# Kernel tuning notes

Measured on AMD Instinct MI355X. Metric: run time of the kernel, lower is better.

The kernel has to match this reference:

```python
import jax, jax.numpy as jnp
import numpy as np

V = 256; D = 512; H = 4 * 2; L = 4; B = 4; T = 512; ML = 1024
FF = 4 * D; FS = 256; NMEL = 80; PN = 512
H = 8


def _ghost(x, idx, scale, lut):
    # LUT dequant (gather) + per-row scale, then GEMM: y = x @ (lut[idx]*scale).T
    w = lut[idx] * scale
    return x @ w.T


def _ln(x, g, b, eps=1e-5):
    m = jnp.mean(x, axis=-1, keepdims=True)
    v = jnp.var(x, axis=-1, keepdims=True)
    return (x - m) / jnp.sqrt(v + eps) * g + b


def _conv1d(x, w, b, pad):
    # x: [B, C, T], w: [O, I, K]
    y = jax.lax.conv_general_dilated(x, w, (1,), [(pad, pad)],
                                     dimension_numbers=('NCH', 'OIH', 'NCH'))
    return y + b[None, :, None]


def _block(x, ai, asc, ui, usc, di, dsc, g, bb, lut):
    Bq, Tq, C = x.shape
    hd = C // H
    h = _ln(x, g[0], bb[0])
    q = _ghost(h, ai[0], asc[0], lut).reshape(Bq, Tq, H, hd).transpose(0, 2, 1, 3)
    k = _ghost(h, ai[1], asc[1], lut).reshape(Bq, Tq, H, hd).transpose(0, 2, 1, 3)
    v = _ghost(h, ai[2], asc[2], lut).reshape(Bq, Tq, H, hd).transpose(0, 2, 1, 3)
    att = jax.nn.softmax(jnp.einsum('bhqd,bhkd->bhqk', q, k) / float(np.sqrt(hd)), axis=-1)
    o = jnp.einsum('bhqk,bhkd->bhqd', att, v).transpose(0, 2, 1, 3).reshape(Bq, Tq, C)
    x = x + _ghost(o, ai[3], asc[3], lut)
    h = _ln(x, g[1], bb[1])
    h = jax.nn.gelu(_ghost(h, ui, usc, lut), approximate=False)
    return x + _ghost(h, di, dsc, lut)


def _varpred(x, p):
    c1w, c1b, g1, b1, c2w, c2b, g2, b2, lw, lb = p
    h = jax.nn.relu(_conv1d(x.transpose(0, 2, 1), c1w, c1b, 1)).transpose(0, 2, 1)
    h = _ln(h, g1, b1)
    h = jax.nn.relu(_conv1d(h.transpose(0, 2, 1), c2w, c2b, 1)).transpose(0, 2, 1)
    h = _ln(h, g2, b2)
    return (h @ lw.T + lb)[..., 0]


def _length_reg(x, dur, max_len):
    # repeat_interleave via cumsum + searchsorted, padded to fixed max_len
    def one(xi, di):
        c = jnp.cumsum(di)
        frames = jnp.arange(max_len)
        tok = jnp.searchsorted(c, frames, side='right')
        valid = (frames < c[-1]).astype(xi.dtype)[:, None]
        return xi[jnp.clip(tok, 0, xi.shape[0] - 1)] * valid
    return jax.vmap(one)(x, dur)


def _forward(floats, ints):
    (lut, emb_table, pos_table, dec_pos_table,
     e_as, e_us, e_ds, e_g, e_b,
     d_as, d_us, d_ds, d_g, d_b,
     vp_c1w, vp_c1b, vp_g1, vp_b1, vp_c2w, vp_c2b, vp_g2, vp_b2, vp_lw, vp_lb,
     proj_w, proj_b, mel_w, mel_b,
     pn_w1, pn_b1, pn_w2, pn_b2, pn_w3, pn_b3, pn_w4, pn_b4, pn_w5, pn_b5,
     pn_g, pn_bb) = floats
    (text, duration_target, e_ai, e_ui, e_di, d_ai, d_ui, d_di) = ints
    Tq = text.shape[1]
    x = emb_table[text] + pos_table[:Tq]
    for i in range(L):
        x = _block(x, e_ai[i], e_as[i], e_ui[i], e_us[i], e_di[i], e_ds[i], e_g[i], e_b[i], lut)
    vp = lambda j: (vp_c1w[j], vp_c1b[j], vp_g1[j], vp_b1[j], vp_c2w[j], vp_c2b[j],
                    vp_g2[j], vp_b2[j], vp_lw[j], vp_lb[j])
    dur_pred = _varpred(x, vp(0))
    x = _length_reg(x, duration_target, ML)
    pitch = _varpred(x, vp(1))
    x = x + pitch[..., None] * proj_w[0, :, 0] + proj_b[0]
    energy = _varpred(x, vp(2))
    x = x + energy[..., None] * proj_w[1, :, 0] + proj_b[1]
    x = x + dec_pos_table[:ML]
    for i in range(L):
        x = _block(x, d_ai[i], d_as[i], d_ui[i], d_us[i], d_di[i], d_ds[i], d_g[i], d_b[i], lut)
    mel = x @ mel_w.T + mel_b  # [B, ML, 80]
    h = mel.transpose(0, 2, 1)
    inv = float(1.0 / np.sqrt(1.0 + 1e-5))  # BN eval with running mean 0, var 1
    bn = lambda z, j: z * inv * pn_g[j][:, None] + pn_bb[j][:, None]
    for j, (w, b) in enumerate([(pn_w1, pn_b1), (pn_w2, pn_b2), (pn_w3, pn_b3), (pn_w4, pn_b4)]):
        h = jnp.tanh(bn(_conv1d(h, w, b, 2), j))
    h = _conv1d(h, pn_w5, pn_b5, 2)
    mel_post = mel + h.transpose(0, 2, 1)
    return mel, mel_post, dur_pred, pitch, energy


def setup_inputs():
    ks = iter(jax.random.split(jax.random.key(0), 80))
    nk = lambda: next(ks)
    lo, hi = -0.08, 0.08
    lut = jnp.linspace(lo, hi, 256, dtype=jnp.float32)
    def qidx(shape):
        w = jax.random.normal(nk(), shape, dtype=jnp.float32) * 0.02
        return jnp.clip(jnp.round((w - lo) / ((hi - lo) / 255.0)), 0, 255).astype(jnp.int32)
    rn = lambda shape, s=0.02: jax.random.normal(nk(), shape, dtype=jnp.float32) * s
    inp = {
        'text': jax.random.randint(nk(), (B, T), 0, V),
        'duration_target': jax.random.randint(nk(), (B, T), 0, 4),
        'lut': lut,
        'emb_table': rn((V, D)), 'pos_table': rn((1024, D)), 'dec_pos_table': rn((2048, D)),
        'e_ai': qidx((L, 4, D, D)), 'e_as': jnp.ones((L, 4, D, 1)),
        'e_ui': qidx((L, FF, D)), 'e_us': jnp.ones((L, FF, 1)),
        'e_di': qidx((L, D, FF)), 'e_ds': jnp.ones((L, D, 1)),
        'e_g': jnp.ones((L, 2, D)), 'e_b': jnp.zeros((L, 2, D)),
        'd_ai': qidx((L, 4, D, D)), 'd_as': jnp.ones((L, 4, D, 1)),
        'd_ui': qidx((L, FF, D)), 'd_us': jnp.ones((L, FF, 1)),
        'd_di': qidx((L, D, FF)), 'd_ds': jnp.ones((L, D, 1)),
        'd_g': jnp.ones((L, 2, D)), 'd_b': jnp.zeros((L, 2, D)),
        'vp_c1w': rn((3, FS, D, 3)), 'vp_c1b': jnp.zeros((3, FS)),
        'vp_g1': jnp.ones((3, FS)), 'vp_b1': jnp.zeros((3, FS)),
        'vp_c2w': rn((3, FS, FS, 3)), 'vp_c2b': jnp.zeros((3, FS)),
        'vp_g2': jnp.ones((3, FS)), 'vp_b2': jnp.zeros((3, FS)),
        'vp_lw': rn((3, 1, FS)), 'vp_lb': jnp.zeros((3, 1)),
        'proj_w': rn((2, D, 1)), 'proj_b': jnp.zeros((2, D)),
        'mel_w': rn((NMEL, D)), 'mel_b': jnp.zeros((NMEL,)),
        'pn_w1': rn((PN, NMEL, 5)), 'pn_b1': jnp.zeros((PN,)),
        'pn_w2': rn((PN, PN, 5)), 'pn_b2': jnp.zeros((PN,)),
        'pn_w3': rn((PN, PN, 5)), 'pn_b3': jnp.zeros((PN,)),
        'pn_w4': rn((PN, PN, 5)), 'pn_b4': jnp.zeros((PN,)),
        'pn_w5': rn((NMEL, PN, 5)), 'pn_b5': jnp.zeros((NMEL,)),
        'pn_g': jnp.ones((4, PN)), 'pn_bb': jnp.zeros((4, PN)),
    }
    return inp


def reference(text, duration_target, lut, emb_table, pos_table, dec_pos_table,
              e_ai, e_as, e_ui, e_us, e_di, e_ds, e_g, e_b,
              d_ai, d_as, d_ui, d_us, d_di, d_ds, d_g, d_b,
              vp_c1w, vp_c1b, vp_g1, vp_b1, vp_c2w, vp_c2b, vp_g2, vp_b2, vp_lw, vp_lb,
              proj_w, proj_b, mel_w, mel_b,
              pn_w1, pn_b1, pn_w2, pn_b2, pn_w3, pn_b3, pn_w4, pn_b4, pn_w5, pn_b5,
              pn_g, pn_bb):
    floats = (lut, emb_table, pos_table, dec_pos_table,
              e_as, e_us, e_ds, e_g, e_b,
              d_as, d_us, d_ds, d_g, d_b,
              vp_c1w, vp_c1b, vp_g1, vp_b1, vp_c2w, vp_c2b, vp_g2, vp_b2, vp_lw, vp_lb,
              proj_w, proj_b, mel_w, mel_b,
              pn_w1, pn_b1, pn_w2, pn_b2, pn_w3, pn_b3, pn_w4, pn_b4, pn_w5, pn_b5,
              pn_g, pn_bb)
    ints = (text, duration_target, e_ai, e_ui, e_di, d_ai, d_ui, d_di)
    return _forward(floats, ints)
```

## Files before the change

kernel.cpp:

```cpp
#include <hip/hip_runtime.h>
#include <math.h>

#define B_    4
#define T_ENC 512
#define ML_   1024
#define D_    512
#define H_    8
#define HD_   64
#define FF_   2048
#define FS_   256
#define NMEL_ 80
#define PN_   512
#define L_    4
#define QKVSTRIDE_ 2097152

typedef __attribute__((ext_vector_type(8))) short bf16x8;
typedef __attribute__((ext_vector_type(8))) unsigned short u16x8;
typedef __attribute__((ext_vector_type(4))) float f32x4;

__device__ inline unsigned short f2bf(float f) {
    union { float f; unsigned u; } v; v.f = f;
    unsigned r = (v.u + 0x7FFFu + ((v.u >> 16) & 1u)) >> 16;
    return (unsigned short)r;
}

__global__ void embed_kernel(const int* __restrict__ text, const float* __restrict__ emb,
                             const float* __restrict__ pos, float* __restrict__ x) {
    int row = blockIdx.x;
    int t = row % T_ENC;
    int tok = text[row];
    float4 e = ((const float4*)(emb + (size_t)tok * D_))[threadIdx.x];
    float4 p = ((const float4*)(pos + (size_t)t * D_))[threadIdx.x];
    e.x += p.x; e.y += p.y; e.z += p.z; e.w += p.w;
    ((float4*)(x + (size_t)row * D_))[threadIdx.x] = e;
}

__global__ __launch_bounds__(256)
void ln_kernel(const float* __restrict__ x, const float* __restrict__ g,
               const float* __restrict__ b, float* __restrict__ out, int D) {
    int row = blockIdx.x * 4 + (threadIdx.x >> 6);
    int lane = threadIdx.x & 63;
    const float* xr = x + (size_t)row * D;
    float4 vals[2];
    int nit = D >> 8;
    float s = 0.f, q = 0.f;
#pragma unroll 2
    for (int it = 0; it < nit; it++) {
        float4 v = ((const float4*)xr)[lane + it * 64];
        vals[it] = v;
        s += v.x + v.y + v.z + v.w;
        q += v.x * v.x + v.y * v.y + v.z * v.z + v.w * v.w;
    }
#pragma unroll
    for (int off = 32; off; off >>= 1) {
        s += __shfl_xor(s, off);
        q += __shfl_xor(q, off);
    }
    float mean = s / D;
    float var  = q / D - mean * mean;
    float rstd = rsqrtf(var + 1e-5f);
    float* orow = out + (size_t)row * D;
#pragma unroll 2
    for (int it = 0; it < nit; it++) {
        int d4 = lane + it * 64;
        float4 gv = ((const float4*)g)[d4];
        float4 bv = ((const float4*)b)[d4];
        float4 v = vals[it];
        v.x = (v.x - mean) * rstd * gv.x + bv.x;
        v.y = (v.y - mean) * rstd * gv.y + bv.y;
        v.z = (v.z - mean) * rstd * gv.z + bv.z;
        v.w = (v.w - mean) * rstd * gv.w + bv.w;
        ((float4*)orow)[d4] = v;
    }
}

enum { EPI_STORE = 0, EPI_ADD = 1, EPI_GELU = 2, EPI_QKV = 3, EPI_BIAS = 4 };

template<int EPI, bool QUANT>
__global__ __launch_bounds__(256)
void gemm_kernel(const float* __restrict__ X, const void* __restrict__ Wv,
                 const float* __restrict__ lut, const float* __restrict__ scale,
                 const float* __restrict__ bias, float* __restrict__ out,
                 int N, int M, int K, int Ttok, int ldo) {
    __shared__ float Xs[16][68];
    __shared__ float Ws[16][68];
    int tid = threadIdx.x;
    int n0 = blockIdx.x * 64, m0 = blockIdx.y * 64;
    int tx = tid & 15, ty = tid >> 4;
    int nl = tid >> 2, kq = (tid & 3) * 4;
    const float* Xp = X + (size_t)(n0 + nl) * K + kq;
    const float* Wf = (const float*)Wv;
    size_t wrow = (size_t)(m0 + nl) * K + kq;
    bool wok = (m0 + nl) < M;
    float c[4][4] = {{0.f}};
    for (int k0 = 0; k0 < K; k0 += 16) {
        __syncthreads();
        float4 xv = *(const float4*)(Xp + k0);
        float w0, w1, w2, w3;
        if (wok) {
            float4 w4 = *(const float4*)(Wf + wrow + k0);
            w0 = w4.x; w1 = w4.y; w2 = w4.z; w3 = w4.w;
        } else { w0 = w1 = w2 = w3 = 0.f; }
        Xs[kq + 0][nl] = xv.x; Xs[kq + 1][nl] = xv.y; Xs[kq + 2][nl] = xv.z; Xs[kq + 3][nl] = xv.w;
        Ws[kq + 0][nl] = w0;   Ws[kq + 1][nl] = w1;   Ws[kq + 2][nl] = w2;   Ws[kq + 3][nl] = w3;
        __syncthreads();
#pragma unroll
        for (int kk = 0; kk < 16; kk++) {
            float4 a = *(const float4*)&Xs[kk][ty * 4];
            float4 w = *(const float4*)&Ws[kk][tx * 4];
            c[0][0] = fmaf(a.x, w.x, c[0][0]); c[0][1] = fmaf(a.x, w.y, c[0][1]);
            c[0][2] = fmaf(a.x, w.z, c[0][2]); c[0][3] = fmaf(a.x, w.w, c[0][3]);
            c[1][0] = fmaf(a.y, w.x, c[1][0]); c[1][1] = fmaf(a.y, w.y, c[1][1]);
            c[1][2] = fmaf(a.y, w.z, c[1][2]); c[1][3] = fmaf(a.y, w.w, c[1][3]);
            c[2][0] = fmaf(a.z, w.x, c[2][0]); c[2][1] = fmaf(a.z, w.y, c[2][1]);
            c[2][2] = fmaf(a.z, w.z, c[2][2]); c[2][3] = fmaf(a.z, w.w, c[2][3]);
            c[3][0] = fmaf(a.w, w.x, c[3][0]); c[3][1] = fmaf(a.w, w.y, c[3][1]);
            c[3][2] = fmaf(a.w, w.z, c[3][2]); c[3][3] = fmaf(a.w, w.w, c[3][3]);
        }
    }
#pragma unroll
    for (int i = 0; i < 4; i++) {
        int n = n0 + ty * 4 + i;
#pragma unroll
        for (int j = 0; j < 4; j++) {
            int m = m0 + tx * 4 + j;
            float v = c[i][j];
            if (EPI == EPI_BIAS) {
                if (m < M) out[(size_t)n * ldo + m] = v + bias[m];
            } else if (EPI == EPI_STORE) {
                if (m < M) out[(size_t)n * ldo + m] = v;
            }
        }
    }
}

template<int EPI>
__global__ __launch_bounds__(256)
void bgemm_kernel(const float* __restrict__ X, const int* __restrict__ Wi,
                  const float* __restrict__ lut, const float* __restrict__ scale,
                  float* __restrict__ out, int N, int M, int K, int Ttok, int ldo,
                  int qkv_stride) {
    __shared__ unsigned short As[2][128][40];
    __shared__ unsigned short Bs[2][64][40];
    int tid = threadIdx.x;
    int n0 = blockIdx.x * 128, m0 = blockIdx.y * 64;
    float lo = lut[0];
    float step = lut[1] - lut[0];
    int arow = tid >> 1, akh = (tid & 1) * 16;
    int brow = tid >> 2, bkq = (tid & 3) * 8;
    const float* Xp = X + (size_t)(n0 + arow) * K + akh;
    const int*   Wp = Wi + (size_t)(m0 + brow) * K + bkq;
    int lane = tid & 63, wid = tid >> 6;
    int lr = lane & 15, lk = lane >> 4;
    int wr = wid >> 1, wc = wid & 1;

    f32x4 acc[4][2];
#pragma unroll
    for (int i = 0; i < 4; i++)
#pragma unroll
        for (int j = 0; j < 2; j++) { f32x4 z = {0.f, 0.f, 0.f, 0.f}; acc[i][j] = z; }

    float4 a0, a1, a2, a3;
    int4 i0, i1;
    auto loadr = [&](int kb) {
        const float4* xp = (const float4*)(Xp + kb);
        a0 = xp[0]; a1 = xp[1]; a2 = xp[2]; a3 = xp[3];
        const int4* ip = (const int4*)(Wp + kb);
        i0 = ip[0]; i1 = ip[1];
    };
    auto storer = [&](int buf) {
        u16x8 w0, w1;
        w0[0] = f2bf(a0.x); w0[1] = f2bf(a0.y); w0[2] = f2bf(a0.z); w0[3] = f2bf(a0.w);
        w0[4] = f2bf(a1.x); w0[5] = f2bf(a1.y); w0[6] = f2bf(a1.z); w0[7] = f2bf(a1.w);
        w1[0] = f2bf(a2.x); w1[1] = f2bf(a2.y); w1[2] = f2bf(a2.z); w1[3] = f2bf(a2.w);
        w1[4] = f2bf(a3.x); w1[5] = f2bf(a3.y); w1[6] = f2bf(a3.z); w1[7] = f2bf(a3.w);
        *(u16x8*)&As[buf][arow][akh]     = w0;
        *(u16x8*)&As[buf][arow][akh + 8] = w1;
        u16x8 wb;
        wb[0] = f2bf(fmaf((float)i0.x, step, lo)); wb[1] = f2bf(fmaf((float)i0.y, step, lo));
        wb[2] = f2bf(fmaf((float)i0.z, step, lo)); wb[3] = f2bf(fmaf((float)i0.w, step, lo));
        wb[4] = f2bf(fmaf((float)i1.x, step, lo)); wb[5] = f2bf(fmaf((float)i1.y, step, lo));
        wb[6] = f2bf(fmaf((float)i1.z, step, lo)); wb[7] = f2bf(fmaf((float)i1.w, step, lo));
        *(u16x8*)&Bs[buf][brow][bkq] = wb;
    };
    auto compute = [&](int buf) {
        bf16x8 af[4], bfv[2];
#pragma unroll
        for (int i = 0; i < 4; i++)
            af[i] = *(const bf16x8*)&As[buf][64 * wr + 16 * i + lr][lk * 8];
#pragma unroll
        for (int j = 0; j < 2; j++)
            bfv[j] = *(const bf16x8*)&Bs[buf][32 * wc + 16 * j + lr][lk * 8];
#pragma unroll
        for (int i = 0; i < 4; i++)
#pragma unroll
            for (int j = 0; j < 2; j++)
                acc[i][j] = __builtin_amdgcn_mfma_f32_16x16x32_bf16(af[i], bfv[j], acc[i][j], 0, 0, 0);
    };

    loadr(0);
    storer(0);
    int nc = K >> 5;
    for (int c = 0; c < nc; c++) {
        int cur = c & 1;
        __syncthreads();
        bool more = (c + 1 < nc);
        if (more) loadr((c + 1) << 5);
        compute(cur);
        if (more) storer(cur ^ 1);
    }

    float sc[2];
#pragma unroll
    for (int j = 0; j < 2; j++) sc[j] = scale[m0 + 32 * wc + 16 * j + lr];
#pragma unroll
    for (int i = 0; i < 4; i++) {
#pragma unroll
        for (int j = 0; j < 2; j++) {
            int m = m0 + 32 * wc + 16 * j + lr;
#pragma unroll
            for (int r = 0; r < 4; r++) {
                int n = n0 + 64 * wr + 16 * i + lk * 4 + r;
                float v = acc[i][j][r] * sc[j];
                if (EPI == EPI_STORE) {
                    out[(size_t)n * ldo + m] = v;
                } else if (EPI == EPI_ADD) {
                    out[(size_t)n * ldo + m] += v;
                } else if (EPI == EPI_GELU) {
                    out[(size_t)n * ldo + m] = 0.5f * v * (1.0f + erff(v * 0.70710678118654752f));
                } else if (EPI == EPI_QKV) {
                    int mat = m >> 9, h = (m >> 6) & 7, dd = m & 63;
                    int b = n / Ttok, t = n - b * Ttok;
                    out[(size_t)mat * qkv_stride + ((size_t)(b * H_ + h) * Ttok + t) * HD_ + dd] = v;
                }
            }
        }
    }
}

template<int TLEN>
__global__ __launch_bounds__(256)
void fattn_kernel(const float* __restrict__ q, const float* __restrict__ k,
                  const float* __restrict__ v, float* __restrict__ o_out) {
    __shared__ float Qs[64][68];
    __shared__ float KP[64][64];
    __shared__ float Vs[64][64];
    int tid = threadIdx.x;
    int tx = tid & 15, ty = tid >> 4;
    int bh = blockIdx.y;
    int q0 = blockIdx.x * 64;
    const float* Qb = q + ((size_t)bh * TLEN + q0) * HD_;
    const float* Kb = k + (size_t)bh * TLEN * HD_;
    const float* Vb = v + (size_t)bh * TLEN * HD_;
    {
        int r = tid >> 4, f = tid & 15;
#pragma unroll
        for (int it = 0; it < 4; it++) {
            int rr = r + 16 * it;
            float4 t4 = *(const float4*)(Qb + (size_t)rr * HD_ + f * 4);
            *(float4*)&Qs[rr][f * 4] = t4;
        }
    }
    float o[4][4] = {{0.f}};
    float m[4], l[4];
#pragma unroll
    for (int i = 0; i < 4; i++) { m[i] = -3e38f; l[i] = 0.f; }
    __syncthreads();

    for (int c0 = 0; c0 < TLEN; c0 += 64) {
        {
            int c = tid >> 2, fo = tid & 3;
#pragma unroll
            for (int it = 0; it < 4; it++) {
                int f = fo + 4 * it;
                float4 t4 = *(const float4*)(Kb + (size_t)(c0 + c) * HD_ + f * 4);
                KP[f * 4 + 0][c] = t4.x; KP[f * 4 + 1][c] = t4.y;
                KP[f * 4 + 2][c] = t4.z; KP[f * 4 + 3][c] = t4.w;
            }
            int r = tid >> 4, ff = tid & 15;
#pragma unroll
            for (int it = 0; it < 4; it++) {
                int rr = r + 16 * it;
                float4 t4 = *(const float4*)(Vb + (size_t)(c0 + rr) * HD_ + ff * 4);
                *(float4*)&Vs[rr][ff * 4] = t4;
            }
        }
        __syncthreads();
        float s[4][4] = {{0.f}};
        for (int k0 = 0; k0 < 64; k0 += 4) {
            float4 qa[4], kb4[4];
#pragma unroll
            for (int i = 0; i < 4; i++) qa[i] = *(const float4*)&Qs[ty * 4 + i][k0];
#pragma unroll
            for (int kk = 0; kk < 4; kk++) kb4[kk] = *(const float4*)&KP[k0 + kk][tx * 4];
#pragma unroll
            for (int i = 0; i < 4; i++) {
                const float* qf = (const float*)&qa[i];
#pragma unroll
                for (int kk = 0; kk < 4; kk++) {
                    float a = qf[kk];
                    s[i][0] = fmaf(a, kb4[kk].x, s[i][0]);
                    s[i][1] = fmaf(a, kb4[kk].y, s[i][1]);
                    s[i][2] = fmaf(a, kb4[kk].z, s[i][2]);
                    s[i][3] = fmaf(a, kb4[kk].w, s[i][3]);
                }
            }
        }
        __syncthreads();
#pragma unroll
        for (int i = 0; i < 4; i++) {
#pragma unroll
            for (int j = 0; j < 4; j++) s[i][j] *= 0.125f;
            float mx = fmaxf(fmaxf(s[i][0], s[i][1]), fmaxf(s[i][2], s[i][3]));
            mx = fmaxf(mx, __shfl_xor(mx, 1));
            mx = fmaxf(mx, __shfl_xor(mx, 2));
            mx = fmaxf(mx, __shfl_xor(mx, 4));
            mx = fmaxf(mx, __shfl_xor(mx, 8));
            float mn = fmaxf(m[i], mx);
            float f = __expf(m[i] - mn);
            float ps = 0.f;
#pragma unroll
            for (int j = 0; j < 4; j++) { float p = __expf(s[i][j] - mn); s[i][j] = p; ps += p; }
            ps += __shfl_xor(ps, 1);
            ps += __shfl_xor(ps, 2);
            ps += __shfl_xor(ps, 4);
            ps += __shfl_xor(ps, 8);
            l[i] = l[i] * f + ps;
            m[i] = mn;
#pragma unroll
            for (int j = 0; j < 4; j++) o[i][j] *= f;
            *(float4*)&KP[ty * 4 + i][tx * 4] = *(float4*)&s[i][0];
        }
        __syncthreads();
        for (int cc0 = 0; cc0 < 64; cc0 += 4) {
            float4 pa[4], vb4[4];
#pragma unroll
            for (int i = 0; i < 4; i++) pa[i] = *(const float4*)&KP[ty * 4 + i][cc0];
#pragma unroll
            for (int cc = 0; cc < 4; cc++) vb4[cc] = *(const float4*)&Vs[cc0 + cc][tx * 4];
#pragma unroll
            for (int i = 0; i < 4; i++) {
                const float* pf = (const float*)&pa[i];
#pragma unroll
                for (int cc = 0; cc < 4; cc++) {
                    float p = pf[cc];
                    o[i][0] = fmaf(p, vb4[cc].x, o[i][0]);
                    o[i][1] = fmaf(p, vb4[cc].y, o[i][1]);
                    o[i][2] = fmaf(p, vb4[cc].z, o[i][2]);
                    o[i][3] = fmaf(p, vb4[cc].w, o[i][3]);
                }
            }
        }
        __syncthreads();
    }
    int b = bh >> 3, hh = bh & 7;
#pragma unroll
    for (int i = 0; i < 4; i++) {
        float inv = 1.0f / l[i];
        int row = q0 + ty * 4 + i;
        float4 r4;
        r4.x = o[i][0] * inv; r4.y = o[i][1] * inv;
        r4.z = o[i][2] * inv; r4.w = o[i][3] * inv;
        *(float4*)(o_out + ((size_t)(b * TLEN + row)) * D_ + hh * HD_ + tx * 4) = r4;
    }
}

enum { CEPI_NONE = 0, CEPI_RELU = 1, CEPI_TANHBN = 2, CEPI_ADDMEL = 3 };

template<int KW, int IN_TM, int OUT_TM, int EPI, int SPLIT>
__global__ __launch_bounds__(256)
void convgemm_kernel(const float* __restrict__ in, const float* __restrict__ w,
                     const float* __restrict__ bias, const float* __restrict__ bng,
                     const float* __restrict__ bnb, const float* __restrict__ meladd,
                     float* __restrict__ out, int Cin, int Cout, int T, int pstride) {
    constexpr int PAD = KW / 2;
    __shared__ float Xs[16][72];
    __shared__ float Ws[16 * KW][68];
    int tid = threadIdx.x;
    int tx = tid & 15, ty = tid >> 4;
    int ntile = T >> 6;
    int b = blockIdx.x / ntile, tc = blockIdx.x % ntile;
    int t0 = tc * 64;
    int m0 = blockIdx.y * 64;
    int z = (SPLIT > 1) ? blockIdx.z : 0;
    int cstart = z * (Cin / SPLIT), cend = cstart + Cin / SPLIT;
    constexpr int XW = 64 + 2 * PAD;
    constexpr int F4PO = (16 * KW) / 4;
    int o_l = tid >> 2, part = tid & 3;
    bool o_ok = (m0 + o_l) < Cout;

    float acc[4][4];
#pragma unroll
    for (int i = 0; i < 4; i++)
#pragma unroll
        for (int j = 0; j < 4; j++) acc[i][j] = 0.f;

    for (int ci0 = cstart; ci0 < cend; ci0 += 16) {
        __syncthreads();
        {
            const float* wb = w + ((size_t)(m0 + o_l) * Cin + ci0) * KW;
            for (int qq = part; qq < F4PO; qq += 4) {
                float4 t4 = o_ok ? *(const float4*)(wb + qq * 4)
                                 : make_float4(0.f, 0.f, 0.f, 0.f);
                Ws[qq * 4 + 0][o_l] = t4.x; Ws[qq * 4 + 1][o_l] = t4.y;
                Ws[qq * 4 + 2][o_l] = t4.z; Ws[qq * 4 + 3][o_l] = t4.w;
            }
        }
        for (int idx = tid; idx < 16 * XW; idx += 256) {
            int r = idx / XW, ccol = idx - r * XW;
            int t = t0 + ccol - PAD;
            float xv = 0.f;
            if (t >= 0 && t < T)
                xv = (IN_TM == 0) ? in[((size_t)(b * Cin + ci0 + r)) * T + t]
                                  : in[((size_t)(b * T + t)) * Cin + ci0 + r];
            Xs[r][ccol] = xv;
        }
        __syncthreads();
#pragma unroll
        for (int kk = 0; kk < 16; kk++) {
            float xr[8];
            float4 xa = *(const float4*)&Xs[kk][tx * 4];
            float4 xb = *(const float4*)&Xs[kk][tx * 4 + 4];
            xr[0] = xa.x; xr[1] = xa.y; xr[2] = xa.z; xr[3] = xa.w;
            xr[4] = xb.x; xr[5] = xb.y; xr[6] = xb.z; xr[7] = xb.w;
#pragma unroll
            for (int k = 0; k < KW; k++) {
                float4 w4 = *(const float4*)&Ws[kk * KW + k][ty * 4];
                const float* wf = (const float*)&w4;
#pragma unroll
                for (int i = 0; i < 4; i++) {
                    float wv = wf[i];
#pragma unroll
                    for (int j = 0; j < 4; j++)
                        acc[i][j] = fmaf(wv, xr[j + k], acc[i][j]);
                }
            }
        }
    }
    const float inv = 0.99999500003749969f;
#pragma unroll
    for (int i = 0; i < 4; i++) {
        int o = m0 + ty * 4 + i;
        if (o >= Cout) continue;
        if (SPLIT > 1) {
            float* po = out + (size_t)z * pstride;
            if (OUT_TM == 0) {
                float4 v4 = make_float4(acc[i][0], acc[i][1], acc[i][2], acc[i][3]);
                *(float4*)(po + ((size_t)(b * Cout + o)) * T + t0 + tx * 4) = v4;
            } else {
#pragma unroll
                for (int j = 0; j < 4; j++)
                    po[((size_t)(b * T + t0 + tx * 4 + j)) * Cout + o] = acc[i][j];
            }
        } else {
            float bsv = bias[o];
            float g = 0.f, bb = 0.f;
            if (EPI == CEPI_TANHBN) { g = bng[o]; bb = bnb[o]; }
            float vj[4];
#pragma unroll
            for (int j = 0; j < 4; j++) {
                int t = t0 + tx * 4 + j;
                float v = acc[i][j] + bsv;
                if (EPI == CEPI_RELU) {
                    v = fmaxf(v, 0.f);
                } else if (EPI == CEPI_TANHBN) {
                    float zz = v * inv * g + bb;
                    zz = fminf(fmaxf(zz, -15.f), 15.f);
                    float e2 = __expf(2.f * zz);
                    v = (e2 - 1.f) / (e2 + 1.f);
                } else if (EPI == CEPI_ADDMEL) {
                    v += meladd[((size_t)(b * T + t)) * NMEL_ + o];
                }
                vj[j] = v;
            }
            if (OUT_TM == 0) {
                *(float4*)(out + ((size_t)(b * Cout + o)) * T + t0 + tx * 4) =
                    make_float4(vj[0], vj[1], vj[2], vj[3]);
            } else {
#pragma unroll
                for (int j = 0; j < 4; j++)
                    out[((size_t)(b * T + t0 + tx * 4 + j)) * Cout + o] = vj[j];
            }
        }
    }
}

template<int OUT_TM, int EPI>
__global__ __launch_bounds__(256)
void convcomb_kernel(const float* __restrict__ p, int pstride, const float* __restrict__ bias,
                     const float* __restrict__ bng, const float* __restrict__ bnb,
                     const float* __restrict__ meladd, float* __restrict__ out,
                     int Cout, int T, int total) {
    int idx = blockIdx.x * 256 + threadIdx.x;
    if (idx >= total) return;
    float v = p[idx] + p[idx + pstride];
    int o = (OUT_TM == 0) ? (idx / T) % Cout : idx % Cout;
    v += bias[o];
    if (EPI == CEPI_RELU) {
        v = fmaxf(v, 0.f);
    } else if (EPI == CEPI_TANHBN) {
        const float inv = 0.99999500003749969f;
        float zz = v * inv * bng[o] + bnb[o];
        zz = fminf(fmaxf(zz, -15.f), 15.f);
        float e2 = __expf(2.f * zz);
        v = (e2 - 1.f) / (e2 + 1.f);
    } else if (EPI == CEPI_ADDMEL) {
        v += meladd[idx];
    }
    out[idx] = v;
}

__global__ void vplin_kernel(const float* __restrict__ h, const float* __restrict__ lw,
                             const float* __restrict__ lb, float* __restrict__ out, int ntok) {
    int row = blockIdx.x * 4 + (threadIdx.x >> 6);
    int lane = threadIdx.x & 63;
    if (row >= ntok) return;
    const float* hr = h + (size_t)row * FS_;
    float s = 0.f;
    for (int c = lane; c < FS_; c += 64) s += hr[c] * lw[c];
#pragma unroll
    for (int off = 32; off; off >>= 1) s += __shfl_down(s, off);
    if (lane == 0) out[row] = s + lb[0];
}

__global__ void cumsum_kernel(const int* __restrict__ dur, int* __restrict__ cums) {
    __shared__ int c[T_ENC];
    int b = blockIdx.x, tid = threadIdx.x;
    c[tid] = dur[b * T_ENC + tid];
    __syncthreads();
    for (int off = 1; off < T_ENC; off <<= 1) {
        int v = (tid >= off) ? c[tid - off] : 0;
        __syncthreads();
        c[tid] += v;
        __syncthreads();
    }
    cums[b * T_ENC + tid] = c[tid];
}

__global__ void regulate_kernel(const float* __restrict__ xe, const int* __restrict__ cums,
                                float* __restrict__ xd) {
    int row = blockIdx.x;
    int b = row / ML_, f = row % ML_;
    const int* c = cums + b * T_ENC;
    int lo = 0, hi = T_ENC;
    while (lo < hi) { int mid = (lo + hi) >> 1; if (c[mid] <= f) lo = mid + 1; else hi = mid; }
    float valid = (f < c[T_ENC - 1]) ? 1.0f : 0.0f;
    int tok = lo < T_ENC ? lo : T_ENC - 1;
    float4 v = ((const float4*)(xe + ((size_t)(b * T_ENC + tok)) * D_))[threadIdx.x];
    v.x *= valid; v.y *= valid; v.z *= valid; v.w *= valid;
    ((float4*)(xd + (size_t)row * D_))[threadIdx.x] = v;
}

__global__ void addscale_kernel(float* __restrict__ x, const float* __restrict__ sc,
                                const float* __restrict__ pw, const float* __restrict__ pb,
                                const float* __restrict__ pos) {
    int row = blockIdx.x;
    int t = row % ML_;
    float s = sc[row];
    float4* xp = (float4*)(x + (size_t)row * D_);
    float4 v = xp[threadIdx.x];
    float4 w4 = ((const float4*)pw)[threadIdx.x];
    float4 b4 = ((const float4*)pb)[threadIdx.x];
    v.x += s * w4.x + b4.x; v.y += s * w4.y + b4.y;
    v.z += s * w4.z + b4.z; v.w += s * w4.w + b4.w;
    if (pos != nullptr) {
        float4 p4 = ((const float4*)(pos + (size_t)t * D_))[threadIdx.x];
        v.x += p4.x; v.y += p4.y; v.z += p4.z; v.w += p4.w;
    }
    xp[threadIdx.x] = v;
}

extern "C" void kernel_launch(void* const* d_in, const int* in_sizes, int n_in,
                              void* d_out, int out_size, void* d_ws, size_t ws_size,
                              hipStream_t stream) {
    (void)in_sizes; (void)n_in; (void)out_size; (void)ws_size;
    const int*   text = (const int*)d_in[0];
    const int*   durt = (const int*)d_in[1];
    const float* lut  = (const float*)d_in[2];
    const float* emb  = (const float*)d_in[3];
    const float* pos  = (const float*)d_in[4];
    const float* dpos = (const float*)d_in[5];
    const int*   e_ai = (const int*)d_in[6];
    const float* e_as = (const float*)d_in[7];
    const int*   e_ui = (const int*)d_in[8];
    const float* e_us = (const float*)d_in[9];
    const int*   e_di = (const int*)d_in[10];
    const float* e_ds = (const float*)d_in[11];
    const float* e_g  = (const float*)d_in[12];
    const float* e_b  = (const float*)d_in[13];
    const int*   d_ai = (const int*)d_in[14];
    const float* d_as = (const float*)d_in[15];
    const int*   d_ui = (const int*)d_in[16];
    const float* d_us = (const float*)d_in[17];
    const int*   d_di = (const int*)d_in[18];
    const float* d_ds = (const float*)d_in[19];
    const float* d_g  = (const float*)d_in[20];
    const float* d_b  = (const float*)d_in[21];
    const float* vp_c1w = (const float*)d_in[22];
    const float* vp_c1b = (const float*)d_in[23];
    const float* vp_g1  = (const float*)d_in[24];
    const float* vp_b1  = (const float*)d_in[25];
    const float* vp_c2w = (const float*)d_in[26];
    const float* vp_c2b = (const float*)d_in[27];
    const float* vp_g2  = (const float*)d_in[28];
    const float* vp_b2  = (const float*)d_in[29];
    const float* vp_lw  = (const float*)d_in[30];
    const float* vp_lb  = (const float*)d_in[31];
    const float* proj_w = (const float*)d_in[32];
    const float* proj_b = (const float*)d_in[33];
    const float* mel_w  = (const float*)d_in[34];
    const float* mel_b  = (const float*)d_in[35];
    const float* pn_w[5] = {(const float*)d_in[36], (const float*)d_in[38], (const float*)d_in[40],
                            (const float*)d_in[42], (const float*)d_in[44]};
    const float* pn_bv[5] = {(const float*)d_in[37], (const float*)d_in[39], (const float*)d_in[41],
                             (const float*)d_in[43], (const float*)d_in[45]};
    const float* pn_g  = (const float*)d_in[46];
    const float* pn_bb = (const float*)d_in[47];

    float* ws = (float*)d_ws;
    float* xe  = ws;
    float* xd  = ws + 1048576;
    float* h   = ws + 3145728;
    float* qb  = ws + 5242880;
    float* kb  = ws + 7340032;
    float* vb  = ws + 9437184;
    float* ob  = ws + 11534336;
    float* hff = ws + 13631488;
    float* vp1 = ws + 22020096;
    float* vp2 = ws + 23068672;
    int*   cums = (int*)(ws + 24117248);
    float* pn_a = ws + 24119296;
    float* pn_b2f = ws + 26216448;

    float* outp   = (float*)d_out;
    float* mel    = outp;
    float* melp   = outp + 327680;
    float* durp   = outp + 655360;
    float* pitch  = outp + 657408;
    float* energy = outp + 661504;

    embed_kernel<<<B_ * T_ENC, 128, 0, stream>>>(text, emb, pos, xe);

    auto run_block = [&](float* x, int T, int N, const int* ai, const float* as,
                         const int* ui, const float* us, const int* di, const float* ds,
                         const float* g, const float* bv) {
        ln_kernel<<<N / 4, 256, 0, stream>>>(x, g, bv, h, D_);
        dim3 gq3(N / 128, 24);
        bgemm_kernel<EPI_QKV><<<gq3, 256, 0, stream>>>(h, ai, lut, as, qb, N, 3 * D_, D_, T, 0, QKVSTRIDE_);
        if (T == T_ENC) fattn_kernel<512><<<dim3(512 / 64, B_ * H_), 256, 0, stream>>>(qb, kb, vb, ob);
        else            fattn_kernel<1024><<<dim3(1024 / 64, B_ * H_), 256, 0, stream>>>(qb, kb, vb, ob);
        dim3 go(N / 128, D_ / 64);
        bgemm_kernel<EPI_ADD><<<go, 256, 0, stream>>>(ob, ai + 3 * D_ * D_, lut, as + 3 * D_, x, N, D_, D_, 0, D_, 0);
        ln_kernel<<<N / 4, 256, 0, stream>>>(x, g + D_, bv + D_, h, D_);
        dim3 gu(N / 128, FF_ / 64);
        bgemm_kernel<EPI_GELU><<<gu, 256, 0, stream>>>(h, ui, lut, us, hff, N, FF_, D_, 0, FF_, 0);
        dim3 gd(N / 128, D_ / 64);
        bgemm_kernel<EPI_ADD><<<gd, 256, 0, stream>>>(hff, di, lut, ds, x, N, D_, FF_, 0, D_, 0);
    };

    for (int l = 0; l < L_; l++)
        run_block(xe, T_ENC, B_ * T_ENC,
                  e_ai + (size_t)l * 4 * D_ * D_, e_as + (size_t)l * 4 * D_,
                  e_ui + (size_t)l * FF_ * D_,    e_us + (size_t)l * FF_,
                  e_di + (size_t)l * D_ * FF_,    e_ds + (size_t)l * D_,
                  e_g + (size_t)l * 2 * D_,       e_b + (size_t)l * 2 * D_);

    auto run_varpred = [&](const float* x, int T, int j, float* out) {
        int N = B_ * T;
        int ps1 = B_ * FS_ * T;
        dim3 gc1(B_ * (T / 64), FS_ / 64, 2);
        convgemm_kernel<3, 1, 1, CEPI_NONE, 2><<<gc1, 256, 0, stream>>>(
            x, vp_c1w + (size_t)j * FS_ * D_ * 3, nullptr, nullptr, nullptr, nullptr,
            hff, D_, FS_, T, ps1);
        convcomb_kernel<1, CEPI_RELU><<<(ps1 + 255) / 256, 256, 0, stream>>>(
            hff, ps1, vp_c1b + j * FS_, nullptr, nullptr, nullptr, vp1, FS_, T, ps1);
        ln_kernel<<<N / 4, 256, 0, stream>>>(vp1, vp_g1 + j * FS_, vp_b1 + j * FS_, vp2, FS_);
        convgemm_kernel<3, 1, 1, CEPI_NONE, 2><<<gc1, 256, 0, stream>>>(
            vp2, vp_c2w + (size_t)j * FS_ * FS_ * 3, nullptr, nullptr, nullptr, nullptr,
            hff, FS_, FS_, T, ps1);
        convcomb_kernel<1, CEPI_RELU><<<(ps1 + 255) / 256, 256, 0, stream>>>(
            hff, ps1, vp_c2b + j * FS_, nullptr, nullptr, nullptr, vp1, FS_, T, ps1);
        ln_kernel<<<N / 4, 256, 0, stream>>>(vp1, vp_g2 + j * FS_, vp_b2 + j * FS_, vp2, FS_);
        vplin_kernel<<<N / 4, 256, 0, stream>>>(vp2, vp_lw + j * FS_, vp_lb + j, out, N);
    };

    run_varpred(xe, T_ENC, 0, durp);

    cumsum_kernel<<<B_, T_ENC, 0, stream>>>(durt, cums);
    regulate_kernel<<<B_ * ML_, 128, 0, stream>>>(xe, cums, xd);

    run_varpred(xd, ML_, 1, pitch);
    addscale_kernel<<<B_ * ML_, 128, 0, stream>>>(xd, pitch, proj_w, proj_b, nullptr);
    run_varpred(xd, ML_, 2, energy);
    addscale_kernel<<<B_ * ML_, 128, 0, stream>>>(xd, energy, proj_w + D_, proj_b + D_, dpos);

    for (int l = 0; l < L_; l++)
        run_block(xd, ML_, B_ * ML_,
                  d_ai + (size_t)l * 4 * D_ * D_, d_as + (size_t)l * 4 * D_,
                  d_ui + (size_t)l * FF_ * D_,    d_us + (size_t)l * FF_,
                  d_di + (size_t)l * D_ * FF_,    d_ds + (size_t)l * D_,
                  d_g + (size_t)l * 2 * D_,       d_b + (size_t)l * 2 * D_);

    {
        dim3 gm((B_ * ML_) / 64, (NMEL_ + 63) / 64);
        gemm_kernel<EPI_BIAS, false><<<gm, 256, 0, stream>>>(xd, mel_w, nullptr, nullptr, mel_b,
                                                             mel, B_ * ML_, NMEL_, D_, 0, NMEL_);
    }

    {
        int psm = B_ * PN_ * ML_;
        int ps5 = B_ * NMEL_ * ML_;
        dim3 g1(B_ * (ML_ / 64), PN_ / 64);
        convgemm_kernel<5, 1, 0, CEPI_TANHBN, 1><<<g1, 256, 0, stream>>>(
            mel, pn_w[0], pn_bv[0], pn_g, pn_bb, nullptr, pn_a, NMEL_, PN_, ML_, 0);
        dim3 gs(B_ * (ML_ / 64), PN_ / 64, 2);
        convgemm_kernel<5, 0, 0, CEPI_NONE, 2><<<gs, 256, 0, stream>>>(
            pn_a, pn_w[1], nullptr, nullptr, nullptr, nullptr, hff, PN_, PN_, ML_, psm);
        convcomb_kernel<0, CEPI_TANHBN><<<(psm + 255) / 256, 256, 0, stream>>>(
            hff, psm, pn_bv[1], pn_g + PN_, pn_bb + PN_, nullptr, pn_b2f, PN_, ML_, psm);
        convgemm_kernel<5, 0, 0, CEPI_NONE, 2><<<gs, 256, 0, stream>>>(
            pn_b2f, pn_w[2], nullptr, nullptr, nullptr, nullptr, hff, PN_, PN_, ML_, psm);
        convcomb_kernel<0, CEPI_TANHBN><<<(psm + 255) / 256, 256, 0, stream>>>(
            hff, psm, pn_bv[2], pn_g + 2 * PN_, pn_bb + 2 * PN_, nullptr, pn_a, PN_, ML_, psm);
        convgemm_kernel<5, 0, 0, CEPI_NONE, 2><<<gs, 256, 0, stream>>>(
            pn_a, pn_w[3], nullptr, nullptr, nullptr, nullptr, hff, PN_, PN_, ML_, psm);
        convcomb_kernel<0, CEPI_TANHBN><<<(psm + 255) / 256, 256, 0, stream>>>(
            hff, psm, pn_bv[3], pn_g + 3 * PN_, pn_bb + 3 * PN_, nullptr, pn_b2f, PN_, ML_, psm);
        dim3 g5(B_ * (ML_ / 64), (NMEL_ + 63) / 64, 2);
        convgemm_kernel<5, 0, 1, CEPI_NONE, 2><<<g5, 256, 0, stream>>>(
            pn_b2f, pn_w[4], nullptr, nullptr, nullptr, nullptr, hff, PN_, NMEL_, ML_, ps5);
        convcomb_kernel<1, CEPI_ADDMEL><<<(ps5 + 255) / 256, 256, 0, stream>>>(
            hff, ps5, pn_bv[4], nullptr, nullptr, mel, melp, NMEL_, ML_, ps5);
    }
}
```

Measured before the change: 3.416 ms.

## Use bf16 MFMA in flash attention and widen conv GEMM time tiles

The flash-attention kernel now converts Q, K and V to bf16 in shared memory and computes QK^T and PV with 16x16x32 bf16 MFMA instructions instead of scalar fp32 FMAs. V is stored transposed and P is written back to shared memory as bf16. Separately, the conv-GEMM kernel's time tile grows from 64 to 128 per block, with 8 outputs per thread, to reuse weights more and cut blocks. The cost is lower precision in attention and higher register pressure in the conv kernel.

```diff
diff --git a/kernel.cpp b/kernel.cpp
--- a/kernel.cpp
+++ b/kernel.cpp
@@ -242,126 +242,119 @@
 __global__ __launch_bounds__(256)
 void fattn_kernel(const float* __restrict__ q, const float* __restrict__ k,
                   const float* __restrict__ v, float* __restrict__ o_out) {
-    __shared__ float Qs[64][68];
-    __shared__ float KP[64][64];
-    __shared__ float Vs[64][64];
+    __shared__ unsigned short QPs[64][72];
+    __shared__ unsigned short Ks[64][72];
+    __shared__ unsigned short Vt[64][72];
     int tid = threadIdx.x;
-    int tx = tid & 15, ty = tid >> 4;
-    int bh = blockIdx.y;
-    int q0 = blockIdx.x * 64;
+    int lane = tid & 63, wid = tid >> 6;
+    int lr = lane & 15, lk = lane >> 4;
+    int bh = blockIdx.y, q0 = blockIdx.x * 64;
     const float* Qb = q + ((size_t)bh * TLEN + q0) * HD_;
     const float* Kb = k + (size_t)bh * TLEN * HD_;
     const float* Vb = v + (size_t)bh * TLEN * HD_;
+    int sr = tid >> 2, sdq = (tid & 3) * 16;
     {
-        int r = tid >> 4, f = tid & 15;
-#pragma unroll
-        for (int it = 0; it < 4; it++) {
-            int rr = r + 16 * it;
-            float4 t4 = *(const float4*)(Qb + (size_t)rr * HD_ + f * 4);
-            *(float4*)&Qs[rr][f * 4] = t4;
-        }
-    }
-    float o[4][4] = {{0.f}};
+        const float4* qp = (const float4*)(Qb + (size_t)sr * HD_ + sdq);
+        float4 f0 = qp[0], f1 = qp[1], f2 = qp[2], f3 = qp[3];
+        u16x8 h0, h1;
+        h0[0] = f2bf(f0.x); h0[1] = f2bf(f0.y); h0[2] = f2bf(f0.z); h0[3] = f2bf(f0.w);
+        h0[4] = f2bf(f1.x); h0[5] = f2bf(f1.y); h0[6] = f2bf(f1.z); h0[7] = f2bf(f1.w);
+        h1[0] = f2bf(f2.x); h1[1] = f2bf(f2.y); h1[2] = f2bf(f2.z); h1[3] = f2bf(f2.w);
+        h1[4] = f2bf(f3.x); h1[5] = f2bf(f3.y); h1[6] = f2bf(f3.z); h1[7] = f2bf(f3.w);
+        *(u16x8*)&QPs[sr][sdq] = h0;
+        *(u16x8*)&QPs[sr][sdq + 8] = h1;
+    }
+    __syncthreads();
+    bf16x8 aq0 = *(const bf16x8*)&QPs[wid * 16 + lr][lk * 8];
+    bf16x8 aq1 = *(const bf16x8*)&QPs[wid * 16 + lr][32 + lk * 8];
     float m[4], l[4];
-#pragma unroll
-    for (int i = 0; i < 4; i++) { m[i] = -3e38f; l[i] = 0.f; }
-    __syncthreads();
+    f32x4 oacc[4];
+#pragma unroll
+    for (int i = 0; i < 4; i++) {
+        m[i] = -3e38f; l[i] = 0.f;
+        f32x4 z = {0.f, 0.f, 0.f, 0.f}; oacc[i] = z;
+    }
 
     for (int c0 = 0; c0 < TLEN; c0 += 64) {
+        __syncthreads();
         {
-            int c = tid >> 2, fo = tid & 3;
-#pragma unroll
-            for (int it = 0; it < 4; it++) {
-                int f = fo + 4 * it;
-                float4 t4 = *(const float4*)(Kb + (size_t)(c0 + c) * HD_ + f * 4);
-                KP[f * 4 + 0][c] = t4.x; KP[f * 4 + 1][c] = t4.y;
-                KP[f * 4 + 2][c] = t4.z; KP[f * 4 + 3][c] = t4.w;
-            }
-            int r = tid >> 4, ff = tid & 15;
-#pragma unroll
-            for (int it = 0; it < 4; it++) {
-                int rr = r + 16 * it;
-                float4 t4 = *(const float4*)(Vb + (size_t)(c0 + rr) * HD_ + ff * 4);
-                *(float4*)&Vs[rr][ff * 4] = t4;
-            }
-        }
-        __syncthreads();
-        float s[4][4] = {{0.f}};
-        for (int k0 = 0; k0 < 64; k0 += 4) {
-            float4 qa[4], kb4[4];
-#pragma unroll
-            for (int i = 0; i < 4; i++) qa[i] = *(const float4*)&Qs[ty * 4 + i][k0];
-#pragma unroll
-            for (int kk = 0; kk < 4; kk++) kb4[kk] = *(const float4*)&KP[k0 + kk][tx * 4];
-#pragma unroll
-            for (int i = 0; i < 4; i++) {
-                const float* qf = (const float*)&qa[i];
-#pragma unroll
-                for (int kk = 0; kk < 4; kk++) {
-                    float a = qf[kk];
-                    s[i][0] = fmaf(a, kb4[kk].x, s[i][0]);
-                    s[i][1] = fmaf(a, kb4[kk].y, s[i][1]);
-                    s[i][2] = fmaf(a, kb4[kk].z, s[i][2]);
-                    s[i][3] = fmaf(a, kb4[kk].w, s[i][3]);
-                }
-            }
-        }
-        __syncthreads();
-#pragma unroll
-        for (int i = 0; i < 4; i++) {
-#pragma unroll
-            for (int j = 0; j < 4; j++) s[i][j] *= 0.125f;
-            float mx = fmaxf(fmaxf(s[i][0], s[i][1]), fmaxf(s[i][2], s[i][3]));
+            const float4* kp = (const float4*)(Kb + (size_t)(c0 + sr) * HD_ + sdq);
+            float4 f0 = kp[0], f1 = kp[1], f2 = kp[2], f3 = kp[3];
+            u16x8 h0, h1;
+            h0[0] = f2bf(f0.x); h0[1] = f2bf(f0.y); h0[2] = f2bf(f0.z); h0[3] = f2bf(f0.w);
+            h0[4] = f2bf(f1.x); h0[5] = f2bf(f1.y); h0[6] = f2bf(f1.z); h0[7] = f2bf(f1.w);
+            h1[0] = f2bf(f2.x); h1[1] = f2bf(f2.y); h1[2] = f2bf(f2.z); h1[3] = f2bf(f2.w);
+            h1[4] = f2bf(f3.x); h1[5] = f2bf(f3.y); h1[6] = f2bf(f3.z); h1[7] = f2bf(f3.w);
+            *(u16x8*)&Ks[sr][sdq] = h0;
+            *(u16x8*)&Ks[sr][sdq + 8] = h1;
+            const float4* vp = (const float4*)(Vb + (size_t)(c0 + sr) * HD_ + sdq);
+            float4 g0 = vp[0], g1 = vp[1], g2 = vp[2], g3 = vp[3];
+            Vt[sdq + 0][sr] = f2bf(g0.x);  Vt[sdq + 1][sr] = f2bf(g0.y);
+            Vt[sdq + 2][sr] = f2bf(g0.z);  Vt[sdq + 3][sr] = f2bf(g0.w);
+            Vt[sdq + 4][sr] = f2bf(g1.x);  Vt[sdq + 5][sr] = f2bf(g1.y);
+            Vt[sdq + 6][sr] = f2bf(g1.z);  Vt[sdq + 7][sr] = f2bf(g1.w);
+            Vt[sdq + 8][sr] = f2bf(g2.x);  Vt[sdq + 9][sr] = f2bf(g2.y);
+            Vt[sdq + 10][sr] = f2bf(g2.z); Vt[sdq + 11][sr] = f2bf(g2.w);
+            Vt[sdq + 12][sr] = f2bf(g3.x); Vt[sdq + 13][sr] = f2bf(g3.y);
+            Vt[sdq + 14][sr] = f2bf(g3.z); Vt[sdq + 15][sr] = f2bf(g3.w);
+        }
+        __syncthreads();
+        f32x4 s[4];
+#pragma unroll
+        for (int n = 0; n < 4; n++) { f32x4 z = {0.f, 0.f, 0.f, 0.f}; s[n] = z; }
+#pragma unroll
+        for (int n = 0; n < 4; n++) {
+            bf16x8 b0 = *(const bf16x8*)&Ks[n * 16 + lr][lk * 8];
+            bf16x8 b1 = *(const bf16x8*)&Ks[n * 16 + lr][32 + lk * 8];
+            s[n] = __builtin_amdgcn_mfma_f32_16x16x32_bf16(aq0, b0, s[n], 0, 0, 0);
+            s[n] = __builtin_amdgcn_mfma_f32_16x16x32_bf16(aq1, b1, s[n], 0, 0, 0);
+        }
+#pragma unroll
+        for (int reg = 0; reg < 4; reg++) {
+            float sv0 = s[0][reg] * 0.125f, sv1 = s[1][reg] * 0.125f;
+            float sv2 = s[2][reg] * 0.125f, sv3 = s[3][reg] * 0.125f;
+            float mx = fmaxf(fmaxf(sv0, sv1), fmaxf(sv2, sv3));
             mx = fmaxf(mx, __shfl_xor(mx, 1));
             mx = fmaxf(mx, __shfl_xor(mx, 2));
             mx = fmaxf(mx, __shfl_xor(mx, 4));
             mx = fmaxf(mx, __shfl_xor(mx, 8));
-            float mn = fmaxf(m[i], mx);
-            float f = __expf(m[i] - mn);
-            float ps = 0.f;
-#pragma unroll
-            for (int j = 0; j < 4; j++) { float p = __expf(s[i][j] - mn); s[i][j] = p; ps += p; }
+            float mn = fmaxf(m[reg], mx);
+            float f = __expf(m[reg] - mn);
+            float p0 = __expf(sv0 - mn), p1 = __expf(sv1 - mn);
+            float p2 = __expf(sv2 - mn), p3 = __expf(sv3 - mn);
+            float ps = p0 + p1 + p2 + p3;
             ps += __shfl_xor(ps, 1);
             ps += __shfl_xor(ps, 2);
             ps += __shfl_xor(ps, 4);
             ps += __shfl_xor(ps, 8);
-            l[i] = l[i] * f + ps;
-            m[i] = mn;
-#pragma unroll
-            for (int j = 0; j < 4; j++) o[i][j] *= f;
-            *(float4*)&KP[ty * 4 + i][tx * 4] = *(float4*)&s[i][0];
-        }
-        __syncthreads();
-        for (int cc0 = 0; cc0 < 64; cc0 += 4) {
-            float4 pa[4], vb4[4];
-#pragma unroll
-            for (int i = 0; i < 4; i++) pa[i] = *(const float4*)&KP[ty * 4 + i][cc0];
-#pragma unroll
-            for (int cc = 0; cc < 4; cc++) vb4[cc] = *(const float4*)&Vs[cc0 + cc][tx * 4];
-#pragma unroll
-            for (int i = 0; i < 4; i++) {
-                const float* pf = (const float*)&pa[i];
-#pragma unroll
-                for (int cc = 0; cc < 4; cc++) {
-                    float p = pf[cc];
-                    o[i][0] = fmaf(p, vb4[cc].x, o[i][0]);
-                    o[i][1] = fmaf(p, vb4[cc].y, o[i][1]);
-                    o[i][2] = fmaf(p, vb4[cc].z, o[i][2]);
-                    o[i][3] = fmaf(p, vb4[cc].w, o[i][3]);
-                }
-            }
-        }
-        __syncthreads();
+            l[reg] = l[reg] * f + ps;
+            m[reg] = mn;
+#pragma unroll
+            for (int n = 0; n < 4; n++) oacc[n][reg] *= f;
+            int prow = wid * 16 + 4 * lk + reg;
+            QPs[prow][0 * 16 + lr] = f2bf(p0);
+            QPs[prow][1 * 16 + lr] = f2bf(p1);
+            QPs[prow][2 * 16 + lr] = f2bf(p2);
+            QPs[prow][3 * 16 + lr] = f2bf(p3);
+        }
+        bf16x8 pa0 = *(const bf16x8*)&QPs[wid * 16 + lr][lk * 8];
+        bf16x8 pa1 = *(const bf16x8*)&QPs[wid * 16 + lr][32 + lk * 8];
+#pragma unroll
+        for (int n = 0; n < 4; n++) {
+            bf16x8 vb0 = *(const bf16x8*)&Vt[n * 16 + lr][lk * 8];
+            bf16x8 vb1 = *(const bf16x8*)&Vt[n * 16 + lr][32 + lk * 8];
+            oacc[n] = __builtin_amdgcn_mfma_f32_16x16x32_bf16(pa0, vb0, oacc[n], 0, 0, 0);
+            oacc[n] = __builtin_amdgcn_mfma_f32_16x16x32_bf16(pa1, vb1, oacc[n], 0, 0, 0);
+        }
     }
     int b = bh >> 3, hh = bh & 7;
 #pragma unroll
-    for (int i = 0; i < 4; i++) {
-        float inv = 1.0f / l[i];
-        int row = q0 + ty * 4 + i;
-        float4 r4;
-        r4.x = o[i][0] * inv; r4.y = o[i][1] * inv;
-        r4.z = o[i][2] * inv; r4.w = o[i][3] * inv;
-        *(float4*)(o_out + ((size_t)(b * TLEN + row)) * D_ + hh * HD_ + tx * 4) = r4;
+    for (int reg = 0; reg < 4; reg++) {
+        float inv = 1.0f / l[reg];
+        int row = q0 + wid * 16 + 4 * lk + reg;
+        float* orow = o_out + ((size_t)(b * TLEN + row)) * D_ + hh * HD_;
+#pragma unroll
+        for (int n = 0; n < 4; n++) orow[n * 16 + lr] = oacc[n][reg] * inv;
     }
 }
 
@@ -374,26 +367,26 @@
                      const float* __restrict__ bnb, const float* __restrict__ meladd,
                      float* __restrict__ out, int Cin, int Cout, int T, int pstride) {
     constexpr int PAD = KW / 2;
-    __shared__ float Xs[16][72];
+    constexpr int XW = 128 + 2 * PAD;
+    __shared__ float Xs[16][136];
     __shared__ float Ws[16 * KW][68];
     int tid = threadIdx.x;
     int tx = tid & 15, ty = tid >> 4;
-    int ntile = T >> 6;
+    int ntile = T >> 7;
     int b = blockIdx.x / ntile, tc = blockIdx.x % ntile;
-    int t0 = tc * 64;
+    int t0 = tc * 128;
     int m0 = blockIdx.y * 64;
     int z = (SPLIT > 1) ? blockIdx.z : 0;
     int cstart = z * (Cin / SPLIT), cend = cstart + Cin / SPLIT;
-    constexpr int XW = 64 + 2 * PAD;
     constexpr int F4PO = (16 * KW) / 4;
     int o_l = tid >> 2, part = tid & 3;
     bool o_ok = (m0 + o_l) < Cout;
 
-    float acc[4][4];
+    float acc[4][8];
 #pragma unroll
     for (int i = 0; i < 4; i++)
 #pragma unroll
-        for (int j = 0; j < 4; j++) acc[i][j] = 0.f;
+        for (int j = 0; j < 8; j++) acc[i][j] = 0.f;
 
     for (int ci0 = cstart; ci0 < cend; ci0 += 16) {
         __syncthreads();
@@ -418,11 +411,13 @@
         __syncthreads();
 #pragma unroll
         for (int kk = 0; kk < 16; kk++) {
-            float xr[8];
-            float4 xa = *(const float4*)&Xs[kk][tx * 4];
-            float4 xb = *(const float4*)&Xs[kk][tx * 4 + 4];
-            xr[0] = xa.x; xr[1] = xa.y; xr[2] = xa.z; xr[3] = xa.w;
-            xr[4] = xb.x; xr[5] = xb.y; xr[6] = xb.z; xr[7] = xb.w;
+            float xr[12];
+            float4 x0 = *(const float4*)&Xs[kk][tx * 8];
+            float4 x1 = *(const float4*)&Xs[kk][tx * 8 + 4];
+            float4 x2 = *(const float4*)&Xs[kk][tx * 8 + 8];
+            xr[0] = x0.x; xr[1] = x0.y; xr[2]  = x0.z; xr[3]  = x0.w;
+            xr[4] = x1.x; xr[5] = x1.y; xr[6]  = x1.z; xr[7]  = x1.w;
+            xr[8] = x2.x; xr[9] = x2.y; xr[10] = x2.z; xr[11] = x2.w;
 #pragma unroll
             for (int k = 0; k < KW; k++) {
                 float4 w4 = *(const float4*)&Ws[kk * KW + k][ty * 4];
@@ -431,7 +426,7 @@
                 for (int i = 0; i < 4; i++) {
                     float wv = wf[i];
 #pragma unroll
-                    for (int j = 0; j < 4; j++)
+                    for (int j = 0; j < 8; j++)
                         acc[i][j] = fmaf(wv, xr[j + k], acc[i][j]);
                 }
             }
@@ -445,21 +440,23 @@
         if (SPLIT > 1) {
             float* po = out + (size_t)z * pstride;
             if (OUT_TM == 0) {
-                float4 v4 = make_float4(acc[i][0], acc[i][1], acc[i][2], acc[i][3]);
-                *(float4*)(po + ((size_t)(b * Cout + o)) * T + t0 + tx * 4) = v4;
+                *(float4*)(po + ((size_t)(b * Cout + o)) * T + t0 + tx * 8) =
+                    make_float4(acc[i][0], acc[i][1], acc[i][2], acc[i][3]);
+                *(float4*)(po + ((size_t)(b * Cout + o)) * T + t0 + tx * 8 + 4) =
+                    make_float4(acc[i][4], acc[i][5], acc[i][6], acc[i][7]);
             } else {
 #pragma unroll
-                for (int j = 0; j < 4; j++)
-                    po[((size_t)(b * T + t0 + tx * 4 + j)) * Cout + o] = acc[i][j];
+                for (int j = 0; j < 8; j++)
+                    po[((size_t)(b * T + t0 + tx * 8 + j)) * Cout + o] = acc[i][j];
             }
         } else {
             float bsv = bias[o];
             float g = 0.f, bb = 0.f;
             if (EPI == CEPI_TANHBN) { g = bng[o]; bb = bnb[o]; }
-            float vj[4];
-#pragma unroll
-            for (int j = 0; j < 4; j++) {
-                int t = t0 + tx * 4 + j;
+            float vj[8];
+#pragma unroll
+            for (int j = 0; j < 8; j++) {
+                int t = t0 + tx * 8 + j;
                 float v = acc[i][j] + bsv;
                 if (EPI == CEPI_RELU) {
                     v = fmaxf(v, 0.f);
@@ -474,12 +471,14 @@
                 vj[j] = v;
             }
             if (OUT_TM == 0) {
-                *(float4*)(out + ((size_t)(b * Cout + o)) * T + t0 + tx * 4) =
+                *(float4*)(out + ((size_t)(b * Cout + o)) * T + t0 + tx * 8) =
                     make_float4(vj[0], vj[1], vj[2], vj[3]);
+                *(float4*)(out + ((size_t)(b * Cout + o)) * T + t0 + tx * 8 + 4) =
+                    make_float4(vj[4], vj[5], vj[6], vj[7]);
             } else {
 #pragma unroll
-                for (int j = 0; j < 4; j++)
-                    out[((size_t)(b * T + t0 + tx * 4 + j)) * Cout + o] = vj[j];
+                for (int j = 0; j < 8; j++)
+                    out[((size_t)(b * T + t0 + tx * 8 + j)) * Cout + o] = vj[j];
             }
         }
     }
@@ -668,7 +667,7 @@
     auto run_varpred = [&](const float* x, int T, int j, float* out) {
         int N = B_ * T;
         int ps1 = B_ * FS_ * T;
-        dim3 gc1(B_ * (T / 64), FS_ / 64, 2);
+        dim3 gc1(B_ * (T / 128), FS_ / 64, 2);
         convgemm_kernel<3, 1, 1, CEPI_NONE, 2><<<gc1, 256, 0, stream>>>(
             x, vp_c1w + (size_t)j * FS_ * D_ * 3, nullptr, nullptr, nullptr, nullptr,
             hff, D_, FS_, T, ps1);
@@ -710,10 +709,10 @@
     {
         int psm = B_ * PN_ * ML_;
         int ps5 = B_ * NMEL_ * ML_;
-        dim3 g1(B_ * (ML_ / 64), PN_ / 64);
+        dim3 g1(B_ * (ML_ / 128), PN_ / 64);
         convgemm_kernel<5, 1, 0, CEPI_TANHBN, 1><<<g1, 256, 0, stream>>>(
             mel, pn_w[0], pn_bv[0], pn_g, pn_bb, nullptr, pn_a, NMEL_, PN_, ML_, 0);
-        dim3 gs(B_ * (ML_ / 64), PN_ / 64, 2);
+        dim3 gs(B_ * (ML_ / 128), PN_ / 64, 2);
         convgemm_kernel<5, 0, 0, CEPI_NONE, 2><<<gs, 256, 0, stream>>>(
             pn_a, pn_w[1], nullptr, nullptr, nullptr, nullptr, hff, PN_, PN_, ML_, psm);
         convcomb_kernel<0, CEPI_TANHBN><<<(psm + 255) / 256, 256, 0, stream>>>(
@@ -726,7 +725,7 @@
             pn_a, pn_w[3], nullptr, nullptr, nullptr, nullptr, hff, PN_, PN_, ML_, psm);
         convcomb_kernel<0, CEPI_TANHBN><<<(psm + 255) / 256, 256, 0, stream>>>(
             hff, psm, pn_bv[3], pn_g + 3 * PN_, pn_bb + 3 * PN_, nullptr, pn_b2f, PN_, ML_, psm);
-        dim3 g5(B_ * (ML_ / 64), (NMEL_ + 63) / 64, 2);
+        dim3 g5(B_ * (ML_ / 128), (NMEL_ + 63) / 64, 2);
         convgemm_kernel<5, 0, 1, CEPI_NONE, 2><<<g5, 256, 0, stream>>>(
             pn_b2f, pn_w[4], nullptr, nullptr, nullptr, nullptr, hff, PN_, NMEL_, ML_, ps5);
         convcomb_kernel<1, CEPI_ADDMEL><<<(ps5 + 255) / 256, 256, 0, stream>>>(
```

Measured after the change: 3.510 ms. 2.8% more time.
